# Optimization experiments

Measured on AMD Instinct MI355X. Metric: run time of the kernel, lower is better.

## Reference

```python
import jax, jax.numpy as jnp
import numpy as np
from jax import lax

POOL = 4  # hp['gcn_pool_size']


def sparsemax(z):
    # sparsemax along last axis (Martins & Astudillo 2016), matches tfa.activations.sparsemax
    n = z.shape[-1]
    z_sorted = jnp.flip(jnp.sort(z, axis=-1), axis=-1)          # descending
    k = jnp.arange(1, n + 1, dtype=z.dtype)
    zcum = jnp.cumsum(z_sorted, axis=-1)
    support = (1.0 + k * z_sorted) > zcum                        # [.., n] bool
    k_sel = jnp.sum(support, axis=-1, keepdims=True)             # int, >= 1
    tau = (jnp.take_along_axis(zcum, k_sel - 1, axis=-1) - 1.0) / k_sel.astype(z.dtype)
    return jnp.maximum(z - tau, 0.0)


def gcn_layer(x, W):
    # x: [B, T, E]
    T = x.shape[1]
    # einsum('Bte,bte->tBb') then mean over t == contract over t,e and divide by T
    adj = jnp.einsum('Bte,bte->Bb', x, x) / T                    # [B, B]
    adj = sparsemax(adj)                                         # row-wise sparsemax
    m = adj[:, :, None, None] * x[None]                          # [B, b, T, E] outer product
    # MaxPool2D((POOL,1), stride 1, 'same') on [batch=B, H=b, W=T, C=E]: pool over neighbor axis b
    m = lax.reduce_window(m, -jnp.inf, lax.max,
                          (1, POOL, 1, 1), (1, 1, 1, 1), 'SAME')
    agg = jnp.sum(m, axis=1)                                     # [B, T, E]
    return jax.nn.relu(agg @ W)                                  # [B, T, rel_dim]


def setup_inputs() -> dict:
    key = jax.random.key(0)
    k0, k1, k2, k3 = jax.random.split(key, 4)
    B, T, E = 64, 256, 64
    rel_dim, n_stack = 4, 8
    x = jax.random.normal(k0, (B, T, E), dtype=jnp.float32)
    W0 = jax.random.normal(k1, (E, rel_dim), dtype=jnp.float32) * 0.1
    W1 = jax.random.normal(k2, (rel_dim, rel_dim), dtype=jnp.float32) * 0.1
    Wp = jax.random.normal(k3, (rel_dim, n_stack), dtype=jnp.float32) * 0.1
    return {"x": x, "W0": W0, "W1": W1, "Wp": Wp}


def reference(x, W0, W1, Wp):
    x = gcn_layer(x, W0)           # layer 0: E -> rel_dim
    x = gcn_layer(x, W1)           # layer 1: rel_dim -> rel_dim
    pooled = jnp.mean(x, axis=1)   # [B, rel_dim], mean over T
    return jax.nn.softmax(pooled @ Wp, axis=-1)  # [B, n_stack]
```

## Files before the change

### kernel.cpp

```cpp
#include <hip/hip_runtime.h>
#include <math.h>

#define B_N 64
#define T_N 256
#define E_N 64
#define R_N 4
#define S_N 8

__device__ __forceinline__ float4 f4max(float4 a, float4 b) {
    return make_float4(fmaxf(a.x, b.x), fmaxf(a.y, b.y), fmaxf(a.z, b.z), fmaxf(a.w, b.w));
}
__device__ __forceinline__ float4 f4scale(float s, float4 v) {
    return make_float4(s * v.x, s * v.y, s * v.z, s * v.w);
}
__device__ __forceinline__ float4 f4add(float4 a, float4 b) {
    return make_float4(a.x + b.x, a.y + b.y, a.z + b.z, a.w + b.w);
}
__device__ __forceinline__ float4 f4fma(float a, float4 b, float4 c) {
    return make_float4(fmaf(a, b.x, c.x), fmaf(a, b.y, c.y), fmaf(a, b.z, c.z), fmaf(a, b.w, c.w));
}

__global__ void gram_partial(const float* __restrict__ X, float* __restrict__ P, int L) {
    __shared__ float xsT[64][68];
    int tid = threadIdx.x;
    int k0 = blockIdx.x * 64;
#pragma unroll
    for (int it = 0; it < 4; ++it) {
        int f = it * 256 + tid;
        int i = f >> 4;
        int k4 = (f & 15) * 4;
        float4 v = *(const float4*)(X + (size_t)i * L + k0 + k4);
        xsT[k4 + 0][i] = v.x; xsT[k4 + 1][i] = v.y;
        xsT[k4 + 2][i] = v.z; xsT[k4 + 3][i] = v.w;
    }
    __syncthreads();
    int ti = (tid >> 4) * 4;
    int tj = (tid & 15) * 4;
    float4 acc0 = make_float4(0, 0, 0, 0), acc1 = acc0, acc2 = acc0, acc3 = acc0;
#pragma unroll 8
    for (int k = 0; k < 64; ++k) {
        float4 a = *(const float4*)&xsT[k][ti];
        float4 b = *(const float4*)&xsT[k][tj];
        acc0 = f4fma(a.x, b, acc0);
        acc1 = f4fma(a.y, b, acc1);
        acc2 = f4fma(a.z, b, acc2);
        acc3 = f4fma(a.w, b, acc3);
    }
    float* base = P + ((size_t)blockIdx.x << 12);
    *(float4*)(base + (ti + 0) * 64 + tj) = acc0;
    *(float4*)(base + (ti + 1) * 64 + tj) = acc1;
    *(float4*)(base + (ti + 2) * 64 + tj) = acc2;
    *(float4*)(base + (ti + 3) * 64 + tj) = acc3;
}

__global__ void reduce_sparsemax(const float* __restrict__ P, float* __restrict__ adj,
                                 int NC, float scale) {
    __shared__ float red[4][64];
    int tid = threadIdx.x;
    int row = blockIdx.x;
    int w = tid >> 6;
    int lane = tid & 63;
    int cpw = NC >> 2;
    float s = 0.f;
    for (int c = w * cpw; c < (w + 1) * cpw; ++c)
        s += P[((size_t)c << 12) + row * 64 + lane];
    red[w][lane] = s;
    __syncthreads();
    if (tid < 64) {
        float z = (red[0][lane] + red[1][lane] + red[2][lane] + red[3][lane]) * scale;
        float v = z;
        for (int k = 2; k <= 64; k <<= 1) {
            bool desc = (lane & k) == 0;
            for (int j = k >> 1; j > 0; j >>= 1) {
                float other = __shfl_xor(v, j, 64);
                bool lower = (lane & j) == 0;
                float mn = fminf(v, other), mx = fmaxf(v, other);
                v = (desc ^ lower) ? mn : mx;
            }
        }
        float c = v;
        for (int d = 1; d < 64; d <<= 1) {
            float n = __shfl_up(c, d, 64);
            if (lane >= d) c += n;
        }
        bool sup = (1.0f + (float)(lane + 1) * v) > c;
        int ksel = __popcll(__ballot(sup));
        float zk = __shfl(c, ksel - 1, 64);
        float tau = (zk - 1.0f) / (float)ksel;
        adj[row * 64 + lane] = fmaxf(z - tau, 0.f);
    }
}

__global__ void agg0_kernel(const float* __restrict__ x, const float* __restrict__ adj,
                            const float* __restrict__ W0, float* __restrict__ h0) {
    __shared__ float xs[64 * 4 * 64];
    int tid = threadIdx.x;
    int t0 = (blockIdx.x >> 3) * 4;
    int Bc = (blockIdx.x & 7) * 8;
#pragma unroll
    for (int it = 0; it < 16; ++it) {
        int f = it * 256 + tid;
        int b = f >> 6;
        int tt = (f >> 4) & 3;
        int e4 = (f & 15) * 4;
        *(float4*)&xs[(b * 4 + tt) * 64 + e4] =
            *(const float4*)(x + ((size_t)(b * 256 + t0 + tt) * 64 + e4));
    }
    __syncthreads();
    int w = __builtin_amdgcn_readfirstlane(tid >> 6);
    int lane = tid & 63;
    int t = lane >> 4;
    int eq = lane & 15;
    const float* pA = adj + (Bc + w * 2) * 64;
    const float* pB = pA + 64;
    float4 w0r0 = *(const float4*)(W0 + (eq * 4 + 0) * 4);
    float4 w0r1 = *(const float4*)(W0 + (eq * 4 + 1) * 4);
    float4 w0r2 = *(const float4*)(W0 + (eq * 4 + 2) * 4);
    float4 w0r3 = *(const float4*)(W0 + (eq * 4 + 3) * 4);
    const float4* xsp = (const float4*)xs;
    const float4 NEG = make_float4(-INFINITY, -INFINITY, -INFINITY, -INFINITY);
    float4 accA = make_float4(0, 0, 0, 0), accB = accA;
    float4 x4 = xsp[(0 * 4 + t) * 16 + eq];
    float4 amA = NEG, a0A = f4scale(pA[0], x4), amB = NEG, a0B = f4scale(pB[0], x4);
    x4 = xsp[(1 * 4 + t) * 16 + eq];
    float4 a1A = f4scale(pA[1], x4), a1B = f4scale(pB[1], x4);
#pragma unroll 8
    for (int bl = 2; bl < 64; ++bl) {
        x4 = xsp[(bl * 4 + t) * 16 + eq];
        float4 v2A = f4scale(pA[bl], x4);
        float4 v2B = f4scale(pB[bl], x4);
        accA = f4add(accA, f4max(f4max(amA, a0A), f4max(a1A, v2A)));
        accB = f4add(accB, f4max(f4max(amB, a0B), f4max(a1B, v2B)));
        amA = a0A; a0A = a1A; a1A = v2A;
        amB = a0B; a0B = a1B; a1B = v2B;
    }
    accA = f4add(accA, f4max(f4max(amA, a0A), a1A));
    accB = f4add(accB, f4max(f4max(amB, a0B), a1B));
    accA = f4add(accA, f4max(a0A, a1A));
    accB = f4add(accB, f4max(a0B, a1B));
#pragma unroll
    for (int half = 0; half < 2; ++half) {
        float4 acc = half ? accB : accA;
        int B = Bc + w * 2 + half;
        float4 h = f4fma(acc.x, w0r0, f4fma(acc.y, w0r1,
                   f4fma(acc.z, w0r2, f4scale(acc.w, w0r3))));
        for (int m = 1; m <= 8; m <<= 1) {
            h.x += __shfl_xor(h.x, m, 64);
            h.y += __shfl_xor(h.y, m, 64);
            h.z += __shfl_xor(h.z, m, 64);
            h.w += __shfl_xor(h.w, m, 64);
        }
        if (eq == 0) {
            float4 r = make_float4(fmaxf(h.x, 0.f), fmaxf(h.y, 0.f),
                                   fmaxf(h.z, 0.f), fmaxf(h.w, 0.f));
            *(float4*)(h0 + (size_t)(B * 256 + t0 + t) * 4) = r;
        }
    }
}

__global__ void agg1_kernel(const float* __restrict__ h0, const float* __restrict__ adj,
                            const float* __restrict__ W1, float* __restrict__ h1) {
    int tid = threadIdx.x;
    int Bi = blockIdx.x >> 2;
    int w = __builtin_amdgcn_readfirstlane(tid >> 6);
    int tb = ((blockIdx.x & 3) * 4 + w) * 16;
    int lane = tid & 63;
    const float* prow = adj + Bi * 64;
    const float* xb = h0 + (size_t)tb * 4 + lane;
    float acc = 0.f;
    float am = -INFINITY;
    float a0 = prow[0] * xb[0];
    float a1 = prow[1] * xb[1024];
#pragma unroll 8
    for (int bl = 2; bl < 64; ++bl) {
        float v2 = prow[bl] * xb[(size_t)bl * 1024];
        acc += fmaxf(fmaxf(am, a0), fmaxf(a1, v2));
        am = a0; a0 = a1; a1 = v2;
    }
    acc += fmaxf(fmaxf(am, a0), a1);
    acc += fmaxf(a0, a1);
    int base = lane & ~3;
    int rc = lane & 3;
    float b0 = __shfl(acc, base + 0, 64);
    float b1 = __shfl(acc, base + 1, 64);
    float b2 = __shfl(acc, base + 2, 64);
    float b3 = __shfl(acc, base + 3, 64);
    float h = b0 * W1[0 * 4 + rc] + b1 * W1[1 * 4 + rc]
            + b2 * W1[2 * 4 + rc] + b3 * W1[3 * 4 + rc];
    h1[(size_t)(Bi * 256 + tb) * 4 + lane] = fmaxf(h, 0.f);
}

__global__ void final_kernel(const float* __restrict__ h1, const float* __restrict__ Wp,
                             float* __restrict__ out) {
    int Bi = blockIdx.x;
    int lane = threadIdx.x;
    const float* hb = h1 + (size_t)Bi * T_N * R_N;
    float acc = 0.f;
    for (int k = lane; k < T_N * R_N; k += 64) acc += hb[k];
    for (int m = 32; m >= 4; m >>= 1) acc += __shfl_xor(acc, m, 64);
    float pooled = acc * (1.0f / (float)T_N);
    float q0 = __shfl(pooled, 0, 64);
    float q1 = __shfl(pooled, 1, 64);
    float q2 = __shfl(pooled, 2, 64);
    float q3 = __shfl(pooled, 3, 64);
    float logit = -INFINITY;
    if (lane < 8)
        logit = q0 * Wp[0 * S_N + lane] + q1 * Wp[1 * S_N + lane]
              + q2 * Wp[2 * S_N + lane] + q3 * Wp[3 * S_N + lane];
    float mx = logit;
    for (int m = 4; m >= 1; m >>= 1) mx = fmaxf(mx, __shfl_xor(mx, m, 8));
    float e = (lane < 8) ? __expf(logit - mx) : 0.f;
    float s = e;
    for (int m = 4; m >= 1; m >>= 1) s += __shfl_xor(s, m, 8);
    if (lane < 8) out[Bi * S_N + lane] = e / s;
}

extern "C" void kernel_launch(void* const* d_in, const int* in_sizes, int n_in,
                              void* d_out, int out_size, void* d_ws, size_t ws_size,
                              hipStream_t stream) {
    const float* x  = (const float*)d_in[0];
    const float* W0 = (const float*)d_in[1];
    const float* W1 = (const float*)d_in[2];
    const float* Wp = (const float*)d_in[3];
    float* out = (float*)d_out;

    char* ws = (char*)d_ws;
    float* P    = (float*)(ws);
    float* adj0 = (float*)(ws + 4194304);
    float* h0   = (float*)(ws + 4194304 + 16384);
    float* adj1 = (float*)(ws + 4194304 + 16384 + 262144);
    float* h1   = (float*)(ws + 4194304 + 2 * 16384 + 262144);

    const float invT = 1.0f / (float)T_N;
    gram_partial<<<256, 256, 0, stream>>>(x, P, T_N * E_N);
    reduce_sparsemax<<<64, 256, 0, stream>>>(P, adj0, 256, invT);
    agg0_kernel<<<512, 256, 0, stream>>>(x, adj0, W0, h0);
    gram_partial<<<16, 256, 0, stream>>>(h0, P, T_N * R_N);
    reduce_sparsemax<<<64, 256, 0, stream>>>(P, adj1, 16, invT);
    agg1_kernel<<<256, 256, 0, stream>>>(h0, adj1, W1, h1);
    final_kernel<<<64, 64, 0, stream>>>(h1, Wp, out);
}
```

Measured before the change: 119.0 us.

## Fuse all stages into one persistent kernel with software grid barriers

New measurement: 301.5 us. 153% more time.

```diff
diff --git a/kernel.cpp b/kernel.cpp
--- a/kernel.cpp
+++ b/kernel.cpp
@@ -1,11 +1,7 @@
 #include <hip/hip_runtime.h>
 #include <math.h>
 
-#define B_N 64
-#define T_N 256
-#define E_N 64
-#define R_N 4
-#define S_N 8
+#define NBLK 256
 
 __device__ __forceinline__ float4 f4max(float4 a, float4 b) {
     return make_float4(fmaxf(a.x, b.x), fmaxf(a.y, b.y), fmaxf(a.z, b.z), fmaxf(a.w, b.w));
@@ -19,200 +15,249 @@
 __device__ __forceinline__ float4 f4fma(float a, float4 b, float4 c) {
     return make_float4(fmaf(a, b.x, c.x), fmaf(a, b.y, c.y), fmaf(a, b.z, c.z), fmaf(a, b.w, c.w));
 }
-
-__global__ void gram_partial(const float* __restrict__ X, float* __restrict__ P, int L) {
-    __shared__ float xsT[64][68];
-    int tid = threadIdx.x;
-    int k0 = blockIdx.x * 64;
-#pragma unroll
-    for (int it = 0; it < 4; ++it) {
-        int f = it * 256 + tid;
-        int i = f >> 4;
-        int k4 = (f & 15) * 4;
-        float4 v = *(const float4*)(X + (size_t)i * L + k0 + k4);
-        xsT[k4 + 0][i] = v.x; xsT[k4 + 1][i] = v.y;
-        xsT[k4 + 2][i] = v.z; xsT[k4 + 3][i] = v.w;
-    }
+__device__ __forceinline__ float4 f4fma4(float4 a, float4 b, float4 c) {
+    return make_float4(fmaf(a.x, b.x, c.x), fmaf(a.y, b.y, c.y),
+                       fmaf(a.z, b.z, c.z), fmaf(a.w, b.w, c.w));
+}
+
+__device__ __forceinline__ void grid_barrier(int* counter, int* gen) {
     __syncthreads();
-    int ti = (tid >> 4) * 4;
-    int tj = (tid & 15) * 4;
-    float4 acc0 = make_float4(0, 0, 0, 0), acc1 = acc0, acc2 = acc0, acc3 = acc0;
-#pragma unroll 8
-    for (int k = 0; k < 64; ++k) {
-        float4 a = *(const float4*)&xsT[k][ti];
-        float4 b = *(const float4*)&xsT[k][tj];
-        acc0 = f4fma(a.x, b, acc0);
-        acc1 = f4fma(a.y, b, acc1);
-        acc2 = f4fma(a.z, b, acc2);
-        acc3 = f4fma(a.w, b, acc3);
-    }
-    float* base = P + ((size_t)blockIdx.x << 12);
-    *(float4*)(base + (ti + 0) * 64 + tj) = acc0;
-    *(float4*)(base + (ti + 1) * 64 + tj) = acc1;
-    *(float4*)(base + (ti + 2) * 64 + tj) = acc2;
-    *(float4*)(base + (ti + 3) * 64 + tj) = acc3;
-}
-
-__global__ void reduce_sparsemax(const float* __restrict__ P, float* __restrict__ adj,
-                                 int NC, float scale) {
-    __shared__ float red[4][64];
-    int tid = threadIdx.x;
-    int row = blockIdx.x;
-    int w = tid >> 6;
-    int lane = tid & 63;
-    int cpw = NC >> 2;
-    float s = 0.f;
-    for (int c = w * cpw; c < (w + 1) * cpw; ++c)
-        s += P[((size_t)c << 12) + row * 64 + lane];
-    red[w][lane] = s;
+    if (threadIdx.x == 0) {
+        __threadfence();
+        int g = __hip_atomic_load(gen, __ATOMIC_RELAXED, __HIP_MEMORY_SCOPE_AGENT);
+        int t = __hip_atomic_fetch_add(counter, 1, __ATOMIC_ACQ_REL, __HIP_MEMORY_SCOPE_AGENT);
+        if (t == NBLK - 1) {
+            __hip_atomic_store(counter, 0, __ATOMIC_RELAXED, __HIP_MEMORY_SCOPE_AGENT);
+            __hip_atomic_fetch_add(gen, 1, __ATOMIC_RELEASE, __HIP_MEMORY_SCOPE_AGENT);
+        } else {
+            while (__hip_atomic_load(gen, __ATOMIC_ACQUIRE, __HIP_MEMORY_SCOPE_AGENT) == g)
+                __builtin_amdgcn_s_sleep(2);
+        }
+        __threadfence();
+    }
     __syncthreads();
-    if (tid < 64) {
-        float z = (red[0][lane] + red[1][lane] + red[2][lane] + red[3][lane]) * scale;
-        float v = z;
-        for (int k = 2; k <= 64; k <<= 1) {
-            bool desc = (lane & k) == 0;
-            for (int j = k >> 1; j > 0; j >>= 1) {
-                float other = __shfl_xor(v, j, 64);
-                bool lower = (lane & j) == 0;
-                float mn = fminf(v, other), mx = fmaxf(v, other);
-                v = (desc ^ lower) ? mn : mx;
+}
+
+__device__ __forceinline__ float wave_sparsemax(float z, int lane) {
+    float v = z;
+    for (int k = 2; k <= 64; k <<= 1) {
+        bool desc = (lane & k) == 0;
+        for (int j = k >> 1; j > 0; j >>= 1) {
+            float other = __shfl_xor(v, j, 64);
+            bool lower = (lane & j) == 0;
+            float mn = fminf(v, other), mx = fmaxf(v, other);
+            v = (desc ^ lower) ? mn : mx;
+        }
+    }
+    float c = v;
+    for (int d = 1; d < 64; d <<= 1) {
+        float n = __shfl_up(c, d, 64);
+        if (lane >= d) c += n;
+    }
+    bool sup = (1.0f + (float)(lane + 1) * v) > c;
+    int ksel = __popcll(__ballot(sup));
+    float zk = __shfl(c, ksel - 1, 64);
+    float tau = (zk - 1.0f) / (float)ksel;
+    return fmaxf(z - tau, 0.f);
+}
+
+__global__ __launch_bounds__(256)
+void mono_kernel(const float* __restrict__ x, const float* __restrict__ W0,
+                 const float* __restrict__ W1, const float* __restrict__ Wp,
+                 float* __restrict__ out, float* __restrict__ P,
+                 float* __restrict__ adj0, float* __restrict__ h0,
+                 float* __restrict__ adj1, int* __restrict__ bar) {
+    __shared__ __align__(16) float smem[16384];
+    const int tid = threadIdx.x;
+    const int lane = tid & 63;
+    const int bid = blockIdx.x;
+    int* counter = bar;
+    int* gen = bar + 1;
+
+    {
+        float (*xsT)[68] = (float (*)[68])smem;
+        int k0 = bid * 64;
+#pragma unroll
+        for (int it = 0; it < 4; ++it) {
+            int f = it * 256 + tid;
+            int i = f >> 4, k4 = (f & 15) * 4;
+            float4 v = *(const float4*)(x + (size_t)i * 16384 + k0 + k4);
+            xsT[k4 + 0][i] = v.x; xsT[k4 + 1][i] = v.y;
+            xsT[k4 + 2][i] = v.z; xsT[k4 + 3][i] = v.w;
+        }
+        __syncthreads();
+        int ti = (tid >> 4) * 4, tj = (tid & 15) * 4;
+        float4 a0 = make_float4(0, 0, 0, 0), a1 = a0, a2 = a0, a3 = a0;
+#pragma unroll 8
+        for (int k = 0; k < 64; ++k) {
+            float4 a = *(const float4*)&xsT[k][ti];
+            float4 b = *(const float4*)&xsT[k][tj];
+            a0 = f4fma(a.x, b, a0); a1 = f4fma(a.y, b, a1);
+            a2 = f4fma(a.z, b, a2); a3 = f4fma(a.w, b, a3);
+        }
+        float* basep = P + ((size_t)bid << 12);
+        *(float4*)(basep + (ti + 0) * 64 + tj) = a0;
+        *(float4*)(basep + (ti + 1) * 64 + tj) = a1;
+        *(float4*)(basep + (ti + 2) * 64 + tj) = a2;
+        *(float4*)(basep + (ti + 3) * 64 + tj) = a3;
+    }
+    grid_barrier(counter, gen);
+
+    if (bid < 64) {
+        float* red = smem;
+        int w = tid >> 6;
+        float s = 0.f;
+        for (int c = w * 64; c < (w + 1) * 64; ++c)
+            s += P[((size_t)c << 12) + bid * 64 + lane];
+        red[w * 64 + lane] = s;
+        __syncthreads();
+        if (tid < 64) {
+            float z = (red[lane] + red[64 + lane] + red[128 + lane] + red[192 + lane])
+                      * (1.0f / 256.0f);
+            adj0[bid * 64 + lane] = wave_sparsemax(z, lane);
+        }
+    }
+    grid_barrier(counter, gen);
+
+    {
+        int t0 = (bid >> 2) * 4;
+        int BcB = (bid & 3) * 16;
+#pragma unroll
+        for (int it = 0; it < 16; ++it) {
+            int f = it * 256 + tid;
+            int b = f >> 6, tt = (f >> 4) & 3, e4 = (f & 15) * 4;
+            *(float4*)&smem[(b * 4 + tt) * 64 + e4] =
+                *(const float4*)(x + ((size_t)(b * 256 + t0 + tt) * 64 + e4));
+        }
+        __syncthreads();
+        int w = __builtin_amdgcn_readfirstlane(tid >> 6);
+        int t = lane >> 4, eq = lane & 15;
+        float4 w0r0 = *(const float4*)(W0 + (eq * 4 + 0) * 4);
+        float4 w0r1 = *(const float4*)(W0 + (eq * 4 + 1) * 4);
+        float4 w0r2 = *(const float4*)(W0 + (eq * 4 + 2) * 4);
+        float4 w0r3 = *(const float4*)(W0 + (eq * 4 + 3) * 4);
+        const float4* xsp = (const float4*)smem;
+#pragma unroll
+        for (int pass = 0; pass < 2; ++pass) {
+            int Bp = BcB + pass * 8 + w * 2;
+            const float* pA = adj0 + Bp * 64;
+            const float* pB = pA + 64;
+            float4 x4 = xsp[(0 * 4 + t) * 16 + eq];
+            float4 vA = f4scale(pA[0], x4), vB = f4scale(pB[0], x4);
+            float4 qm1A = vA, qm1B = vB;
+            x4 = xsp[(1 * 4 + t) * 16 + eq];
+            float4 vtA = f4scale(pA[1], x4), vtB = f4scale(pB[1], x4);
+            float4 qbA = f4max(vA, vtA), qbB = f4max(vB, vtB);
+            float4 accA = make_float4(0, 0, 0, 0), accB = accA;
+#pragma unroll 8
+            for (int bl = 0; bl < 62; ++bl) {
+                x4 = xsp[((bl + 2) * 4 + t) * 16 + eq];
+                float4 vnA = f4scale(pA[bl + 2], x4);
+                float4 vnB = f4scale(pB[bl + 2], x4);
+                float4 q1A = f4max(vtA, vnA), q1B = f4max(vtB, vnB);
+                accA = f4add(accA, f4max(qm1A, q1A));
+                accB = f4add(accB, f4max(qm1B, q1B));
+                qm1A = qbA; qbA = q1A; vtA = vnA;
+                qm1B = qbB; qbB = q1B; vtB = vnB;
             }
-        }
-        float c = v;
-        for (int d = 1; d < 64; d <<= 1) {
-            float n = __shfl_up(c, d, 64);
-            if (lane >= d) c += n;
-        }
-        bool sup = (1.0f + (float)(lane + 1) * v) > c;
-        int ksel = __popcll(__ballot(sup));
-        float zk = __shfl(c, ksel - 1, 64);
-        float tau = (zk - 1.0f) / (float)ksel;
-        adj[row * 64 + lane] = fmaxf(z - tau, 0.f);
-    }
-}
-
-__global__ void agg0_kernel(const float* __restrict__ x, const float* __restrict__ adj,
-                            const float* __restrict__ W0, float* __restrict__ h0) {
-    __shared__ float xs[64 * 4 * 64];
-    int tid = threadIdx.x;
-    int t0 = (blockIdx.x >> 3) * 4;
-    int Bc = (blockIdx.x & 7) * 8;
-#pragma unroll
-    for (int it = 0; it < 16; ++it) {
-        int f = it * 256 + tid;
-        int b = f >> 6;
-        int tt = (f >> 4) & 3;
-        int e4 = (f & 15) * 4;
-        *(float4*)&xs[(b * 4 + tt) * 64 + e4] =
-            *(const float4*)(x + ((size_t)(b * 256 + t0 + tt) * 64 + e4));
-    }
-    __syncthreads();
-    int w = __builtin_amdgcn_readfirstlane(tid >> 6);
-    int lane = tid & 63;
-    int t = lane >> 4;
-    int eq = lane & 15;
-    const float* pA = adj + (Bc + w * 2) * 64;
-    const float* pB = pA + 64;
-    float4 w0r0 = *(const float4*)(W0 + (eq * 4 + 0) * 4);
-    float4 w0r1 = *(const float4*)(W0 + (eq * 4 + 1) * 4);
-    float4 w0r2 = *(const float4*)(W0 + (eq * 4 + 2) * 4);
-    float4 w0r3 = *(const float4*)(W0 + (eq * 4 + 3) * 4);
-    const float4* xsp = (const float4*)xs;
-    const float4 NEG = make_float4(-INFINITY, -INFINITY, -INFINITY, -INFINITY);
-    float4 accA = make_float4(0, 0, 0, 0), accB = accA;
-    float4 x4 = xsp[(0 * 4 + t) * 16 + eq];
-    float4 amA = NEG, a0A = f4scale(pA[0], x4), amB = NEG, a0B = f4scale(pB[0], x4);
-    x4 = xsp[(1 * 4 + t) * 16 + eq];
-    float4 a1A = f4scale(pA[1], x4), a1B = f4scale(pB[1], x4);
-#pragma unroll 8
-    for (int bl = 2; bl < 64; ++bl) {
-        x4 = xsp[(bl * 4 + t) * 16 + eq];
-        float4 v2A = f4scale(pA[bl], x4);
-        float4 v2B = f4scale(pB[bl], x4);
-        accA = f4add(accA, f4max(f4max(amA, a0A), f4max(a1A, v2A)));
-        accB = f4add(accB, f4max(f4max(amB, a0B), f4max(a1B, v2B)));
-        amA = a0A; a0A = a1A; a1A = v2A;
-        amB = a0B; a0B = a1B; a1B = v2B;
-    }
-    accA = f4add(accA, f4max(f4max(amA, a0A), a1A));
-    accB = f4add(accB, f4max(f4max(amB, a0B), a1B));
-    accA = f4add(accA, f4max(a0A, a1A));
-    accB = f4add(accB, f4max(a0B, a1B));
-#pragma unroll
-    for (int half = 0; half < 2; ++half) {
-        float4 acc = half ? accB : accA;
-        int B = Bc + w * 2 + half;
-        float4 h = f4fma(acc.x, w0r0, f4fma(acc.y, w0r1,
-                   f4fma(acc.z, w0r2, f4scale(acc.w, w0r3))));
-        for (int m = 1; m <= 8; m <<= 1) {
-            h.x += __shfl_xor(h.x, m, 64);
-            h.y += __shfl_xor(h.y, m, 64);
-            h.z += __shfl_xor(h.z, m, 64);
-            h.w += __shfl_xor(h.w, m, 64);
-        }
-        if (eq == 0) {
-            float4 r = make_float4(fmaxf(h.x, 0.f), fmaxf(h.y, 0.f),
-                                   fmaxf(h.z, 0.f), fmaxf(h.w, 0.f));
-            *(float4*)(h0 + (size_t)(B * 256 + t0 + t) * 4) = r;
-        }
-    }
-}
-
-__global__ void agg1_kernel(const float* __restrict__ h0, const float* __restrict__ adj,
-                            const float* __restrict__ W1, float* __restrict__ h1) {
-    int tid = threadIdx.x;
-    int Bi = blockIdx.x >> 2;
-    int w = __builtin_amdgcn_readfirstlane(tid >> 6);
-    int tb = ((blockIdx.x & 3) * 4 + w) * 16;
-    int lane = tid & 63;
-    const float* prow = adj + Bi * 64;
-    const float* xb = h0 + (size_t)tb * 4 + lane;
-    float acc = 0.f;
-    float am = -INFINITY;
-    float a0 = prow[0] * xb[0];
-    float a1 = prow[1] * xb[1024];
-#pragma unroll 8
-    for (int bl = 2; bl < 64; ++bl) {
-        float v2 = prow[bl] * xb[(size_t)bl * 1024];
-        acc += fmaxf(fmaxf(am, a0), fmaxf(a1, v2));
-        am = a0; a0 = a1; a1 = v2;
-    }
-    acc += fmaxf(fmaxf(am, a0), a1);
-    acc += fmaxf(a0, a1);
-    int base = lane & ~3;
-    int rc = lane & 3;
-    float b0 = __shfl(acc, base + 0, 64);
-    float b1 = __shfl(acc, base + 1, 64);
-    float b2 = __shfl(acc, base + 2, 64);
-    float b3 = __shfl(acc, base + 3, 64);
-    float h = b0 * W1[0 * 4 + rc] + b1 * W1[1 * 4 + rc]
-            + b2 * W1[2 * 4 + rc] + b3 * W1[3 * 4 + rc];
-    h1[(size_t)(Bi * 256 + tb) * 4 + lane] = fmaxf(h, 0.f);
-}
-
-__global__ void final_kernel(const float* __restrict__ h1, const float* __restrict__ Wp,
-                             float* __restrict__ out) {
-    int Bi = blockIdx.x;
-    int lane = threadIdx.x;
-    const float* hb = h1 + (size_t)Bi * T_N * R_N;
-    float acc = 0.f;
-    for (int k = lane; k < T_N * R_N; k += 64) acc += hb[k];
-    for (int m = 32; m >= 4; m >>= 1) acc += __shfl_xor(acc, m, 64);
-    float pooled = acc * (1.0f / (float)T_N);
-    float q0 = __shfl(pooled, 0, 64);
-    float q1 = __shfl(pooled, 1, 64);
-    float q2 = __shfl(pooled, 2, 64);
-    float q3 = __shfl(pooled, 3, 64);
-    float logit = -INFINITY;
-    if (lane < 8)
-        logit = q0 * Wp[0 * S_N + lane] + q1 * Wp[1 * S_N + lane]
-              + q2 * Wp[2 * S_N + lane] + q3 * Wp[3 * S_N + lane];
-    float mx = logit;
-    for (int m = 4; m >= 1; m >>= 1) mx = fmaxf(mx, __shfl_xor(mx, m, 8));
-    float e = (lane < 8) ? __expf(logit - mx) : 0.f;
-    float s = e;
-    for (int m = 4; m >= 1; m >>= 1) s += __shfl_xor(s, m, 8);
-    if (lane < 8) out[Bi * S_N + lane] = e / s;
+            accA = f4add(accA, f4max(qm1A, vtA));
+            accB = f4add(accB, f4max(qm1B, vtB));
+            accA = f4add(accA, qbA);
+            accB = f4add(accB, qbB);
+#pragma unroll
+            for (int half = 0; half < 2; ++half) {
+                float4 acc = half ? accB : accA;
+                float4 h = f4fma(acc.x, w0r0, f4fma(acc.y, w0r1,
+                           f4fma(acc.z, w0r2, f4scale(acc.w, w0r3))));
+                for (int m = 1; m <= 8; m <<= 1) {
+                    h.x += __shfl_xor(h.x, m, 64);
+                    h.y += __shfl_xor(h.y, m, 64);
+                    h.z += __shfl_xor(h.z, m, 64);
+                    h.w += __shfl_xor(h.w, m, 64);
+                }
+                if (eq == 0) {
+                    float4 r = make_float4(fmaxf(h.x, 0.f), fmaxf(h.y, 0.f),
+                                           fmaxf(h.z, 0.f), fmaxf(h.w, 0.f));
+                    *(float4*)(h0 + (size_t)((Bp + half) * 256 + t0 + t) * 4) = r;
+                }
+            }
+        }
+    }
+    grid_barrier(counter, gen);
+
+    if (bid < 64) {
+        float* row = smem;
+        float* part = smem + 1024;
+        *(float4*)(row + tid * 4) = *(const float4*)(h0 + (size_t)bid * 1024 + tid * 4);
+        __syncthreads();
+        int j = tid >> 2, q = tid & 3;
+        const float4* hj = (const float4*)(h0 + (size_t)j * 1024 + q * 256);
+        const float4* ri = (const float4*)(row + q * 256);
+        float4 s4 = make_float4(0, 0, 0, 0);
+#pragma unroll 8
+        for (int kk = 0; kk < 64; ++kk) s4 = f4fma4(ri[kk], hj[kk], s4);
+        part[tid] = s4.x + s4.y + s4.z + s4.w;
+        __syncthreads();
+        if (tid < 64) {
+            float z = (part[lane * 4] + part[lane * 4 + 1] + part[lane * 4 + 2]
+                       + part[lane * 4 + 3]) * (1.0f / 256.0f);
+            adj1[bid * 64 + lane] = wave_sparsemax(z, lane);
+        }
+    }
+    grid_barrier(counter, gen);
+
+    if (bid < 64) {
+        int w = __builtin_amdgcn_readfirstlane(tid >> 6);
+        int rc = lane & 3;
+        const float* prow = adj1 + bid * 64;
+        float psum = 0.f;
+#pragma unroll
+        for (int gg = 0; gg < 4; ++gg) {
+            int tbase = w * 64 + gg * 16;
+            const float* xb = h0 + (size_t)tbase * 4 + lane;
+            float v0 = prow[0] * xb[0];
+            float v1 = prow[1] * xb[1024];
+            float qm1 = v0, qb = fmaxf(v0, v1), vt = v1, acc = 0.f;
+#pragma unroll 8
+            for (int bl = 0; bl < 62; ++bl) {
+                float vn = prow[bl + 2] * xb[(size_t)(bl + 2) * 1024];
+                float q1 = fmaxf(vt, vn);
+                acc += fmaxf(qm1, q1);
+                qm1 = qb; qb = q1; vt = vn;
+            }
+            acc += fmaxf(qm1, vt);
+            acc += qb;
+            int base = lane & ~3;
+            float b0 = __shfl(acc, base + 0, 64);
+            float b1 = __shfl(acc, base + 1, 64);
+            float b2 = __shfl(acc, base + 2, 64);
+            float b3 = __shfl(acc, base + 3, 64);
+            float h = b0 * W1[rc] + b1 * W1[4 + rc] + b2 * W1[8 + rc] + b3 * W1[12 + rc];
+            psum += fmaxf(h, 0.f);
+        }
+        for (int m = 4; m <= 32; m <<= 1) psum += __shfl_xor(psum, m, 64);
+        __syncthreads();
+        if (lane < 4) smem[w * 4 + lane] = psum;
+        __syncthreads();
+        if (tid < 64) {
+            float pooled = 0.f;
+            if (lane < 4)
+                pooled = (smem[lane] + smem[4 + lane] + smem[8 + lane] + smem[12 + lane])
+                         * (1.0f / 256.0f);
+            float q0 = __shfl(pooled, 0, 64), q1 = __shfl(pooled, 1, 64);
+            float q2 = __shfl(pooled, 2, 64), q3 = __shfl(pooled, 3, 64);
+            float logit = -INFINITY;
+            if (lane < 8)
+                logit = q0 * Wp[lane] + q1 * Wp[8 + lane]
+                      + q2 * Wp[16 + lane] + q3 * Wp[24 + lane];
+            float mx = logit;
+            for (int m = 4; m >= 1; m >>= 1) mx = fmaxf(mx, __shfl_xor(mx, m, 8));
+            float e = (lane < 8) ? __expf(logit - mx) : 0.f;
+            float s = e;
+            for (int m = 4; m >= 1; m >>= 1) s += __shfl_xor(s, m, 8);
+            if (lane < 8) out[bid * 8 + lane] = e / s;
+        }
+    }
 }
 
 extern "C" void kernel_launch(void* const* d_in, const int* in_sizes, int n_in,
@@ -226,17 +271,11 @@
 
     char* ws = (char*)d_ws;
     float* P    = (float*)(ws);
-    float* adj0 = (float*)(ws + 4194304);
-    float* h0   = (float*)(ws + 4194304 + 16384);
-    float* adj1 = (float*)(ws + 4194304 + 16384 + 262144);
-    float* h1   = (float*)(ws + 4194304 + 2 * 16384 + 262144);
-
-    const float invT = 1.0f / (float)T_N;
-    gram_partial<<<256, 256, 0, stream>>>(x, P, T_N * E_N);
-    reduce_sparsemax<<<64, 256, 0, stream>>>(P, adj0, 256, invT);
-    agg0_kernel<<<512, 256, 0, stream>>>(x, adj0, W0, h0);
-    gram_partial<<<16, 256, 0, stream>>>(h0, P, T_N * R_N);
-    reduce_sparsemax<<<64, 256, 0, stream>>>(P, adj1, 16, invT);
-    agg1_kernel<<<256, 256, 0, stream>>>(h0, adj1, W1, h1);
-    final_kernel<<<64, 64, 0, stream>>>(h1, Wp, out);
-}
+    float* adj0 = (float*)(ws + (4u << 20));
+    float* h0   = (float*)(ws + (4u << 20) + 16384);
+    float* adj1 = (float*)(ws + (4u << 20) + 16384 + 262144);
+    int*   bar  = (int*)  (ws + (4u << 20) + 2 * 16384 + 262144);
+
+    hipMemsetAsync(bar, 0, 64, stream);
+    mono_kernel<<<NBLK, 256, 0, stream>>>(x, W0, W1, Wp, out, P, adj0, h0, adj1, bar);
+}
```
